# Kernel tuning notes

Hardware: AMD Instinct MI355X
Metric: run time of the kernel (lower is better)

The kernel has to match this reference:

```python
import jax, jax.numpy as jnp
import numpy as np

EPS = 1e-9  # Dice BatchNorm epsilon

def _dice(x, alpha, mm, mv):
    # Keras BN(center=False, scale=False) in inference mode: (x - moving_mean) / sqrt(moving_var + eps)
    p = jax.nn.sigmoid((x - mm) * jax.lax.rsqrt(mv + EPS))
    return x * (p + alpha * (1.0 - p))

def setup_inputs() -> dict:
    key = jax.random.key(0)
    ks = jax.random.split(key, 8)
    B, T, E = 4096, 200, 12
    return {
        "query": jax.random.normal(ks[0], (B, 1, E), jnp.float32),
        "keys": jax.random.normal(ks[1], (B, T, E), jnp.float32),
        "mask": jnp.ones((B, T), dtype=bool),
        "W0": jax.random.normal(ks[2], (48, 80), jnp.float32) * (1.0 / np.sqrt(48)),
        "b0": jnp.zeros((80,), jnp.float32),
        "W1": jax.random.normal(ks[3], (80, 40), jnp.float32) * (1.0 / np.sqrt(80)),
        "b1": jnp.zeros((40,), jnp.float32),
        "alpha0": jax.random.uniform(ks[4], (80,), jnp.float32),
        "alpha1": jax.random.uniform(ks[5], (40,), jnp.float32),
        "mm0": jnp.zeros((80,), jnp.float32),
        "mv0": jnp.ones((80,), jnp.float32),
        "mm1": jnp.zeros((40,), jnp.float32),
        "mv1": jnp.ones((40,), jnp.float32),
        "atten_kernel": jax.random.normal(ks[6], (40, 1), jnp.float32) * (1.0 / np.sqrt(40)),
        "atten_bias": jnp.zeros((1,), jnp.float32),
    }

def reference(query, keys, mask, W0, b0, W1, b1, alpha0, alpha1,
              mm0, mv0, mm1, mv1, atten_kernel, atten_bias):
    B, T, E = keys.shape
    q = jnp.broadcast_to(query, (B, T, E))  # K.repeat_elements(query, T, 1)
    att = jnp.concatenate([q, keys, q - keys, q * keys], axis=-1)  # [B, T, 4E=48]
    h = _dice(jnp.einsum('bti,io->bto', att, W0) + b0, alpha0, mm0, mv0)  # [B,T,80]
    h = _dice(jnp.einsum('bti,io->bto', h, W1) + b1, alpha1, mm1, mv1)    # [B,T,40]
    score = jnp.einsum('bti,io->bto', h, atten_kernel) + atten_bias       # [B,T,1]
    scores = jnp.swapaxes(score, 1, 2)  # [B,1,T]
    # NOTE: original code computes tf.where(mask,...) but overwrites it and
    # matmuls the UNMASKED scores with keys (bug reproduced faithfully).
    return jnp.matmul(scores, keys)  # [B,1,E]
```

## Files before the change

kernel.cpp:

```cpp
#include <hip/hip_runtime.h>
#include <hip/hip_bf16.h>
#include <math.h>

#define B_TOT 4096
#define T_LEN 200
#define E_DIM 12
#define LOG2E 1.44269504088896340736f

typedef __attribute__((ext_vector_type(8))) short bf16x8;
typedef __attribute__((ext_vector_type(4))) float f32x4;
typedef unsigned short ushort_t;


__device__ inline unsigned short f2bf(float f) {
    union { float f; unsigned u; } x; x.f = f;
    unsigned r = x.u + 0x7FFFu + ((x.u >> 16) & 1u);
    return (unsigned short)(r >> 16);
}
__device__ inline unsigned pk_bf16(float a, float b) {
    float2 t; t.x = a; t.y = b;
    __hip_bfloat162 h = __float22bfloat162_rn(t);
    union { __hip_bfloat162 h; unsigned u; } cv; cv.h = h;
    return cv.u;
}

__global__ __launch_bounds__(256) void din_prep(
    const float* __restrict__ W0, const float* __restrict__ b0v,
    const float* __restrict__ W1, const float* __restrict__ b1v,
    const float* __restrict__ a0, const float* __restrict__ a1,
    const float* __restrict__ mm0, const float* __restrict__ mv0,
    const float* __restrict__ mm1, const float* __restrict__ mv1,
    const float* __restrict__ ak, const float* __restrict__ ab,
    void* __restrict__ wsv)
{
    unsigned char* wsb = (unsigned char*)wsv;
    ushort_t* w0e2 = (ushort_t*)wsb;
    ushort_t* wq   = (ushort_t*)(wsb + 5120);
    ushort_t* w1e  = (ushort_t*)(wsb + 10240);
    float* d0c = (float*)(wsb + 19456);
    float* d1c = (float*)(wsb + 20736);

    int idx = blockIdx.x * 256 + threadIdx.x;
    if (idx < 2560) {
        int n = idx >> 5, k = idx & 31;
        float v = 0.0f;
        if (k < 12)       v = W0[(12 + k) * 80 + n] - W0[(24 + k) * 80 + n];
        else if (k < 24)  v = W0[(36 + (k - 12)) * 80 + n];
        w0e2[n * 32 + k] = f2bf(v);
    } else if (idx < 5120) {
        int v2 = idx - 2560;
        int n = v2 >> 5, k = v2 & 31;
        float v = 0.0f;
        if (k < 12)       v = W0[k * 80 + n] + W0[(24 + k) * 80 + n];
        else if (k == 12) v = b0v[n];
        wq[n * 32 + k] = f2bf(v);
    } else if (idx < 9728) {
        int v2 = idx - 5120;
        int n = v2 / 96, k = v2 - n * 96;
        float v = 0.0f;
        if (n < 40) {
            if (k < 80)       v = W1[k * 40 + n];
            else if (k == 80) v = b1v[n];
        } else if (n == 40 && k == 80) {
            v = 1.0f;
        }
        w1e[n * 96 + k] = f2bf(v);
    } else if (idx < 10048) {
        int v2 = idx - 9728;
        int o = v2 >> 2, c = v2 & 3;
        float rs = rsqrtf(mv0[o] + 1e-9f) * LOG2E;
        float val = (c == 0) ? -rs : (c == 1) ? mm0[o] * rs : (c == 2) ? a0[o] : 1.0f - a0[o];
        d0c[o * 4 + c] = val;
    } else {
        int v2 = idx - 10048;
        int j = v2 >> 2, c = v2 & 3;
        float val = 0.0f;
        if (j < 40) {
            float rs = rsqrtf(mv1[j] + 1e-9f) * LOG2E;
            val = (c == 0) ? -rs : (c == 1) ? mm1[j] * rs : (c == 2) ? a1[j] * ak[j]
                                                          : (1.0f - a1[j]) * ak[j];
        } else if (j == 40 && c == 2) {
            val = ab[0];
        }
        d1c[j * 4 + c] = val;
    }
}

#define A0_STR 40
#define H_STR  104
#define W1_STR 104

__global__ __launch_bounds__(256, 3) void din_mfma(
    const float* __restrict__ query, const float* __restrict__ keys,
    const void* __restrict__ wsv, float* __restrict__ out)
{
    __shared__ __align__(16) ushort_t Aseg[4 * 64];
    __shared__ __align__(16) ushort_t A0[4 * 64 * A0_STR];
    __shared__ __align__(16) ushort_t H[4 * 16 * H_STR];
    __shared__ __align__(16) f32x4 d0cL[80];
    __shared__ __align__(16) f32x4 d1cL[48];
    __shared__ __align__(16) ushort_t w1eL[48 * W1_STR];
    const unsigned char* wsb = (const unsigned char*)wsv;
    const ushort_t* w0e2 = (const ushort_t*)wsb;
    const ushort_t* wq   = (const ushort_t*)(wsb + 5120);
    const ushort_t* w1e  = (const ushort_t*)(wsb + 10240);
    const f32x4* d0cp = (const f32x4*)(wsb + 19456);
    const f32x4* d1cp = (const f32x4*)(wsb + 20736);

    const int tid = threadIdx.x;
    const int lane = tid & 63;
    const int w = tid >> 6;
    const int l15 = lane & 15;
    const int quad = lane >> 4;
    const int b = blockIdx.x * 4 + w;

    ushort_t* A0w = &A0[w * 64 * A0_STR];
    ushort_t* Hw  = &H[w * 16 * H_STR];
    ushort_t* Asw = &Aseg[w * 64];

    if (tid < 80)        d0cL[tid] = d0cp[tid];
    else if (tid < 128)  d1cL[tid - 80] = d1cp[tid - 80];
    for (int idx = tid; idx < 48 * 12; idx += 256) {
        int row = idx / 12, g = idx - row * 12;
        *(uint4*)(w1eL + row * W1_STR + g * 8) =
            *(const uint4*)(w1e + row * 96 + g * 8);
    }

    bf16x8 b0f[5];
    #pragma unroll
    for (int nt = 0; nt < 5; ++nt)
        b0f[nt] = *(const bf16x8*)(w0e2 + (nt * 16 + l15) * 32 + quad * 8);

    float qq[12];
    {
        const float4* qp = (const float4*)(query + (size_t)b * E_DIM);
        float4 q0 = qp[0], q1 = qp[1], q2 = qp[2];
        qq[0]=q0.x; qq[1]=q0.y; qq[2]=q0.z; qq[3]=q0.w;
        qq[4]=q1.x; qq[5]=q1.y; qq[6]=q1.z; qq[7]=q1.w;
        qq[8]=q2.x; qq[9]=q2.y; qq[10]=q2.z; qq[11]=q2.w;
    }

    float z0q[5];
    {
        unsigned p01 = pk_bf16(qq[0], qq[1]), p23 = pk_bf16(qq[2], qq[3]);
        unsigned p45 = pk_bf16(qq[4], qq[5]), p67 = pk_bf16(qq[6], qq[7]);
        unsigned p89 = pk_bf16(qq[8], qq[9]), pab = pk_bf16(qq[10], qq[11]);
        union { unsigned u[4]; bf16x8 v; } qa;
        qa.u[0] = (quad == 0) ? p01 : (quad == 1) ? p89 : 0u;
        qa.u[1] = (quad == 0) ? p23 : (quad == 1) ? pab : 0u;
        qa.u[2] = (quad == 0) ? p45 : (quad == 1) ? 0x00003F80u : 0u;
        qa.u[3] = (quad == 0) ? p67 : 0u;
        #pragma unroll
        for (int nt = 0; nt < 5; ++nt) {
            bf16x8 wf = *(const bf16x8*)(wq + (nt * 16 + l15) * 32 + quad * 8);
            f32x4 zz = {0.f, 0.f, 0.f, 0.f};
            zz = __builtin_amdgcn_mfma_f32_16x16x32_bf16(qa.v, wf, zz, 0, 0, 0);
            z0q[nt] = zz[0];
        }
    }

    if (quad == 0) {
        bf16x8 one8 = {(short)0x3F80, 0, 0, 0, 0, 0, 0, 0};
        bf16x8 zero8 = {0, 0, 0, 0, 0, 0, 0, 0};
        *(bf16x8*)(Hw + l15 * H_STR + 80) = one8;
        *(bf16x8*)(Hw + l15 * H_STR + 88) = zero8;
    }
    {
        uint4 z4; z4.x = 0u; z4.y = 0u; z4.z = 0u; z4.w = 0u;
        ((uint4*)(A0w + lane * A0_STR))[3] = z4;
    }

    __syncthreads();

    f32x4 acc2 = {0.f, 0.f, 0.f, 0.f};

    for (int c = 0; c < 4; ++c) {
        const int t0 = c * 64;
        const int myT = t0 + lane;
        const bool valid = myT < T_LEN;

        float kk[12];
        if (valid) {
            const float4* kp = (const float4*)(keys + ((size_t)b * T_LEN + myT) * E_DIM);
            float4 k0 = kp[0], k1 = kp[1], k2 = kp[2];
            kk[0]=k0.x; kk[1]=k0.y; kk[2]=k0.z; kk[3]=k0.w;
            kk[4]=k1.x; kk[5]=k1.y; kk[6]=k1.z; kk[7]=k1.w;
            kk[8]=k2.x; kk[9]=k2.y; kk[10]=k2.z; kk[11]=k2.w;
        } else {
            #pragma unroll
            for (int i = 0; i < 12; ++i) kk[i] = 0.0f;
        }
        {
            unsigned kw[6], qkw[6];
            #pragma unroll
            for (int i = 0; i < 6; ++i)
                kw[i] = pk_bf16(kk[2 * i], kk[2 * i + 1]);
            #pragma unroll
            for (int i = 0; i < 6; ++i)
                qkw[i] = pk_bf16(qq[2 * i] * kk[2 * i], qq[2 * i + 1] * kk[2 * i + 1]);
            uint4* dst = (uint4*)(A0w + lane * A0_STR);
            uint4 v0, v1, v2;
            v0.x = kw[0];  v0.y = kw[1];  v0.z = kw[2];  v0.w = kw[3];
            v1.x = kw[4];  v1.y = kw[5];  v1.z = qkw[0]; v1.w = qkw[1];
            v2.x = qkw[2]; v2.y = qkw[3]; v2.z = qkw[4]; v2.w = qkw[5];
            dst[0] = v0; dst[1] = v1; dst[2] = v2;
        }

        const int ntiles = (c < 3) ? 4 : 1;
        for (int ti = 0; ti < ntiles; ++ti) {
            bf16x8 a0 = *(const bf16x8*)(A0w + (ti * 16 + l15) * A0_STR + quad * 8);

            #pragma unroll
            for (int nt = 0; nt < 5; ++nt) {
                float zq = z0q[nt];
                f32x4 cc = {zq, zq, zq, zq};
                cc = __builtin_amdgcn_mfma_f32_16x16x32_bf16(a0, b0f[nt], cc, 0, 0, 0);
                f32x4 dc = d0cL[nt * 16 + l15];
                float h[4];
                #pragma unroll
                for (int r = 0; r < 4; ++r) {
                    float z = cc[r];
                    float pg = __builtin_amdgcn_rcpf(
                        1.0f + __builtin_amdgcn_exp2f(fmaf(z, dc.x, dc.y)));
                    h[r] = z * fmaf(pg, dc.w, dc.z);
                }
                unsigned u01 = pk_bf16(h[0], h[1]);
                unsigned u23 = pk_bf16(h[2], h[3]);
                ushort_t* hcol = Hw + (quad * 4) * H_STR + nt * 16 + l15;
                hcol[0 * H_STR] = (ushort_t)u01;
                hcol[1 * H_STR] = (ushort_t)(u01 >> 16);
                hcol[2 * H_STR] = (ushort_t)u23;
                hcol[3 * H_STR] = (ushort_t)(u23 >> 16);
            }

            bf16x8 af[3];
            #pragma unroll
            for (int ks = 0; ks < 3; ++ks)
                af[ks] = *(const bf16x8*)(Hw + l15 * H_STR + ks * 32 + quad * 8);
            float s[4] = {0.f, 0.f, 0.f, 0.f};
            #pragma unroll
            for (int nt = 0; nt < 3; ++nt) {
                f32x4 cc = {0.f, 0.f, 0.f, 0.f};
                #pragma unroll
                for (int ks = 0; ks < 3; ++ks) {
                    bf16x8 bf = *(const bf16x8*)(w1eL + (nt * 16 + l15) * W1_STR
                                                 + ks * 32 + quad * 8);
                    cc = __builtin_amdgcn_mfma_f32_16x16x32_bf16(af[ks], bf, cc, 0, 0, 0);
                }
                f32x4 dc1 = d1cL[nt * 16 + l15];
                #pragma unroll
                for (int r = 0; r < 4; ++r) {
                    float z = cc[r];
                    float pg = __builtin_amdgcn_rcpf(
                        1.0f + __builtin_amdgcn_exp2f(fmaf(z, dc1.x, dc1.y)));
                    s[r] = fmaf(z, fmaf(pg, dc1.w, dc1.z), s[r]);
                }
            }
            #pragma unroll
            for (int m = 1; m < 16; m <<= 1) {
                #pragma unroll
                for (int r = 0; r < 4; ++r) s[r] += __shfl_xor(s[r], m, 64);
            }
            if (l15 == 0) {
                const int tb = t0 + ti * 16 + quad * 4;
                float v0 = (tb + 0 < T_LEN) ? s[0] : 0.0f;
                float v1 = (tb + 1 < T_LEN) ? s[1] : 0.0f;
                float v2 = (tb + 2 < T_LEN) ? s[2] : 0.0f;
                float v3 = (tb + 3 < T_LEN) ? s[3] : 0.0f;
                unsigned lo = pk_bf16(v0, v1), hi = pk_bf16(v2, v3);
                unsigned long long pk = (unsigned long long)lo
                                      | ((unsigned long long)hi << 32);
                *(unsigned long long*)(Asw + ti * 16 + quad * 4) = pk;
            }
        }

        const int nks = (c < 3) ? 2 : 1;
        for (int ks = 0; ks < nks; ++ks) {
            bf16x8 pa = *(const bf16x8*)(Asw + l15 * 64 + ks * 32 + quad * 8);
            bf16x8 bk;
            #pragma unroll
            for (int j = 0; j < 8; ++j)
                bk[j] = (short)A0w[(ks * 32 + quad * 8 + j) * A0_STR + l15];
            acc2 = __builtin_amdgcn_mfma_f32_16x16x32_bf16(pa, bk, acc2, 0, 0, 0);
        }
    }

    if (quad == 0 && l15 < 12)
        out[(size_t)b * E_DIM + l15] = acc2[0];
}

extern "C" void kernel_launch(void* const* d_in, const int* in_sizes, int n_in,
                              void* d_out, int out_size, void* d_ws, size_t ws_size,
                              hipStream_t stream) {
    const float* query = (const float*)d_in[0];
    const float* keys  = (const float*)d_in[1];
    const float* W0  = (const float*)d_in[3];
    const float* b0v = (const float*)d_in[4];
    const float* W1  = (const float*)d_in[5];
    const float* b1v = (const float*)d_in[6];
    const float* a0  = (const float*)d_in[7];
    const float* a1  = (const float*)d_in[8];
    const float* mm0 = (const float*)d_in[9];
    const float* mv0 = (const float*)d_in[10];
    const float* mm1 = (const float*)d_in[11];
    const float* mv1 = (const float*)d_in[12];
    const float* ak  = (const float*)d_in[13];
    const float* ab  = (const float*)d_in[14];
    float* out = (float*)d_out;

    hipLaunchKernelGGL(din_prep, dim3(40), dim3(256), 0, stream,
                       W0, b0v, W1, b1v, a0, a1, mm0, mv0, mm1, mv1, ak, ab, d_ws);
    hipLaunchKernelGGL(din_mfma, dim3(B_TOT / 4), dim3(256), 0, stream,
                       query, keys, d_ws, out);
}
```

Baseline: 150.0 us.

## Process two 16-row tiles per iteration and keep W1 fragments in registers

The tile loop now handles pairs of 16-token tiles, interleaving two independent MFMA and Dice chains to hide MFMA latency. Each wave gets a double-buffered H scratch region. The W1 B-fragments are preloaded into registers instead of being staged in shared memory and re-read every tile. The extra register pressure lowers the launch bound from 3 to 2 blocks per CU, and the last chunk computes a redundant B tile whose result is discarded.

After: 152.5 us. Within noise of the previous version (+1.6%).

```diff
diff --git a/kernel.cpp b/kernel.cpp
--- a/kernel.cpp
+++ b/kernel.cpp
@@ -88,18 +88,16 @@
 
 #define A0_STR 40
 #define H_STR  104
-#define W1_STR 104
-
-__global__ __launch_bounds__(256, 3) void din_mfma(
+
+__global__ __launch_bounds__(256, 2) void din_mfma(
     const float* __restrict__ query, const float* __restrict__ keys,
     const void* __restrict__ wsv, float* __restrict__ out)
 {
     __shared__ __align__(16) ushort_t Aseg[4 * 64];
     __shared__ __align__(16) ushort_t A0[4 * 64 * A0_STR];
-    __shared__ __align__(16) ushort_t H[4 * 16 * H_STR];
+    __shared__ __align__(16) ushort_t H[4 * 2 * 16 * H_STR];
     __shared__ __align__(16) f32x4 d0cL[80];
     __shared__ __align__(16) f32x4 d1cL[48];
-    __shared__ __align__(16) ushort_t w1eL[48 * W1_STR];
     const unsigned char* wsb = (const unsigned char*)wsv;
     const ushort_t* w0e2 = (const ushort_t*)wsb;
     const ushort_t* wq   = (const ushort_t*)(wsb + 5120);
@@ -115,21 +113,23 @@
     const int b = blockIdx.x * 4 + w;
 
     ushort_t* A0w = &A0[w * 64 * A0_STR];
-    ushort_t* Hw  = &H[w * 16 * H_STR];
+    ushort_t* HwA = &H[(w * 2 + 0) * 16 * H_STR];
+    ushort_t* HwB = &H[(w * 2 + 1) * 16 * H_STR];
     ushort_t* Asw = &Aseg[w * 64];
 
     if (tid < 80)        d0cL[tid] = d0cp[tid];
     else if (tid < 128)  d1cL[tid - 80] = d1cp[tid - 80];
-    for (int idx = tid; idx < 48 * 12; idx += 256) {
-        int row = idx / 12, g = idx - row * 12;
-        *(uint4*)(w1eL + row * W1_STR + g * 8) =
-            *(const uint4*)(w1e + row * 96 + g * 8);
-    }
 
     bf16x8 b0f[5];
     #pragma unroll
     for (int nt = 0; nt < 5; ++nt)
         b0f[nt] = *(const bf16x8*)(w0e2 + (nt * 16 + l15) * 32 + quad * 8);
+    bf16x8 b1f[3][3];
+    #pragma unroll
+    for (int nt = 0; nt < 3; ++nt)
+        #pragma unroll
+        for (int ks = 0; ks < 3; ++ks)
+            b1f[nt][ks] = *(const bf16x8*)(w1e + (nt * 16 + l15) * 96 + ks * 32 + quad * 8);
 
     float qq[12];
     {
@@ -162,8 +162,10 @@
     if (quad == 0) {
         bf16x8 one8 = {(short)0x3F80, 0, 0, 0, 0, 0, 0, 0};
         bf16x8 zero8 = {0, 0, 0, 0, 0, 0, 0, 0};
-        *(bf16x8*)(Hw + l15 * H_STR + 80) = one8;
-        *(bf16x8*)(Hw + l15 * H_STR + 88) = zero8;
+        *(bf16x8*)(HwA + l15 * H_STR + 80) = one8;
+        *(bf16x8*)(HwA + l15 * H_STR + 88) = zero8;
+        *(bf16x8*)(HwB + l15 * H_STR + 80) = one8;
+        *(bf16x8*)(HwB + l15 * H_STR + 88) = zero8;
     }
     {
         uint4 z4; z4.x = 0u; z4.y = 0u; z4.z = 0u; z4.w = 0u;
@@ -206,71 +208,106 @@
             dst[0] = v0; dst[1] = v1; dst[2] = v2;
         }
 
-        const int ntiles = (c < 3) ? 4 : 1;
-        for (int ti = 0; ti < ntiles; ++ti) {
-            bf16x8 a0 = *(const bf16x8*)(A0w + (ti * 16 + l15) * A0_STR + quad * 8);
+        const int npairs = (c < 3) ? 2 : 1;
+        for (int pp = 0; pp < npairs; ++pp) {
+            const int tA = 2 * pp;
+            const int tB = (c < 3) ? (2 * pp + 1) : 0;
+            const bool writeB = (c < 3);
+
+            bf16x8 aA = *(const bf16x8*)(A0w + (tA * 16 + l15) * A0_STR + quad * 8);
+            bf16x8 aB = *(const bf16x8*)(A0w + (tB * 16 + l15) * A0_STR + quad * 8);
 
             #pragma unroll
             for (int nt = 0; nt < 5; ++nt) {
                 float zq = z0q[nt];
-                f32x4 cc = {zq, zq, zq, zq};
-                cc = __builtin_amdgcn_mfma_f32_16x16x32_bf16(a0, b0f[nt], cc, 0, 0, 0);
+                f32x4 cA = {zq, zq, zq, zq};
+                f32x4 cB = {zq, zq, zq, zq};
+                cA = __builtin_amdgcn_mfma_f32_16x16x32_bf16(aA, b0f[nt], cA, 0, 0, 0);
+                cB = __builtin_amdgcn_mfma_f32_16x16x32_bf16(aB, b0f[nt], cB, 0, 0, 0);
                 f32x4 dc = d0cL[nt * 16 + l15];
-                float h[4];
+                float hA[4], hB[4];
                 #pragma unroll
                 for (int r = 0; r < 4; ++r) {
-                    float z = cc[r];
-                    float pg = __builtin_amdgcn_rcpf(
-                        1.0f + __builtin_amdgcn_exp2f(fmaf(z, dc.x, dc.y)));
-                    h[r] = z * fmaf(pg, dc.w, dc.z);
-                }
-                unsigned u01 = pk_bf16(h[0], h[1]);
-                unsigned u23 = pk_bf16(h[2], h[3]);
-                ushort_t* hcol = Hw + (quad * 4) * H_STR + nt * 16 + l15;
-                hcol[0 * H_STR] = (ushort_t)u01;
-                hcol[1 * H_STR] = (ushort_t)(u01 >> 16);
-                hcol[2 * H_STR] = (ushort_t)u23;
-                hcol[3 * H_STR] = (ushort_t)(u23 >> 16);
-            }
-
-            bf16x8 af[3];
-            #pragma unroll
-            for (int ks = 0; ks < 3; ++ks)
-                af[ks] = *(const bf16x8*)(Hw + l15 * H_STR + ks * 32 + quad * 8);
-            float s[4] = {0.f, 0.f, 0.f, 0.f};
+                    float zA = cA[r], zB = cB[r];
+                    float pA = __builtin_amdgcn_rcpf(
+                        1.0f + __builtin_amdgcn_exp2f(fmaf(zA, dc.x, dc.y)));
+                    float pB = __builtin_amdgcn_rcpf(
+                        1.0f + __builtin_amdgcn_exp2f(fmaf(zB, dc.x, dc.y)));
+                    hA[r] = zA * fmaf(pA, dc.w, dc.z);
+                    hB[r] = zB * fmaf(pB, dc.w, dc.z);
+                }
+                unsigned a01 = pk_bf16(hA[0], hA[1]), a23 = pk_bf16(hA[2], hA[3]);
+                unsigned b01 = pk_bf16(hB[0], hB[1]), b23 = pk_bf16(hB[2], hB[3]);
+                ushort_t* hcA = HwA + (quad * 4) * H_STR + nt * 16 + l15;
+                ushort_t* hcB = HwB + (quad * 4) * H_STR + nt * 16 + l15;
+                hcA[0 * H_STR] = (ushort_t)a01;
+                hcA[1 * H_STR] = (ushort_t)(a01 >> 16);
+                hcA[2 * H_STR] = (ushort_t)a23;
+                hcA[3 * H_STR] = (ushort_t)(a23 >> 16);
+                hcB[0 * H_STR] = (ushort_t)b01;
+                hcB[1 * H_STR] = (ushort_t)(b01 >> 16);
+                hcB[2 * H_STR] = (ushort_t)b23;
+                hcB[3 * H_STR] = (ushort_t)(b23 >> 16);
+            }
+
+            bf16x8 afA[3], afB[3];
+            #pragma unroll
+            for (int ks = 0; ks < 3; ++ks) {
+                afA[ks] = *(const bf16x8*)(HwA + l15 * H_STR + ks * 32 + quad * 8);
+                afB[ks] = *(const bf16x8*)(HwB + l15 * H_STR + ks * 32 + quad * 8);
+            }
+            float sA[4] = {0.f, 0.f, 0.f, 0.f};
+            float sB[4] = {0.f, 0.f, 0.f, 0.f};
             #pragma unroll
             for (int nt = 0; nt < 3; ++nt) {
-                f32x4 cc = {0.f, 0.f, 0.f, 0.f};
+                f32x4 cA = {0.f, 0.f, 0.f, 0.f};
+                f32x4 cB = {0.f, 0.f, 0.f, 0.f};
                 #pragma unroll
                 for (int ks = 0; ks < 3; ++ks) {
-                    bf16x8 bf = *(const bf16x8*)(w1eL + (nt * 16 + l15) * W1_STR
-                                                 + ks * 32 + quad * 8);
-                    cc = __builtin_amdgcn_mfma_f32_16x16x32_bf16(af[ks], bf, cc, 0, 0, 0);
+                    cA = __builtin_amdgcn_mfma_f32_16x16x32_bf16(afA[ks], b1f[nt][ks], cA, 0, 0, 0);
+                    cB = __builtin_amdgcn_mfma_f32_16x16x32_bf16(afB[ks], b1f[nt][ks], cB, 0, 0, 0);
                 }
                 f32x4 dc1 = d1cL[nt * 16 + l15];
                 #pragma unroll
                 for (int r = 0; r < 4; ++r) {
-                    float z = cc[r];
-                    float pg = __builtin_amdgcn_rcpf(
-                        1.0f + __builtin_amdgcn_exp2f(fmaf(z, dc1.x, dc1.y)));
-                    s[r] = fmaf(z, fmaf(pg, dc1.w, dc1.z), s[r]);
+                    float zA = cA[r], zB = cB[r];
+                    float pA = __builtin_amdgcn_rcpf(
+                        1.0f + __builtin_amdgcn_exp2f(fmaf(zA, dc1.x, dc1.y)));
+                    float pB = __builtin_amdgcn_rcpf(
+                        1.0f + __builtin_amdgcn_exp2f(fmaf(zB, dc1.x, dc1.y)));
+                    sA[r] = fmaf(zA, fmaf(pA, dc1.w, dc1.z), sA[r]);
+                    sB[r] = fmaf(zB, fmaf(pB, dc1.w, dc1.z), sB[r]);
                 }
             }
             #pragma unroll
             for (int m = 1; m < 16; m <<= 1) {
                 #pragma unroll
-                for (int r = 0; r < 4; ++r) s[r] += __shfl_xor(s[r], m, 64);
+                for (int r = 0; r < 4; ++r) {
+                    sA[r] += __shfl_xor(sA[r], m, 64);
+                    sB[r] += __shfl_xor(sB[r], m, 64);
+                }
             }
             if (l15 == 0) {
-                const int tb = t0 + ti * 16 + quad * 4;
-                float v0 = (tb + 0 < T_LEN) ? s[0] : 0.0f;
-                float v1 = (tb + 1 < T_LEN) ? s[1] : 0.0f;
-                float v2 = (tb + 2 < T_LEN) ? s[2] : 0.0f;
-                float v3 = (tb + 3 < T_LEN) ? s[3] : 0.0f;
-                unsigned lo = pk_bf16(v0, v1), hi = pk_bf16(v2, v3);
-                unsigned long long pk = (unsigned long long)lo
-                                      | ((unsigned long long)hi << 32);
-                *(unsigned long long*)(Asw + ti * 16 + quad * 4) = pk;
+                {
+                    const int tb = t0 + tA * 16 + quad * 4;
+                    float v0 = (tb + 0 < T_LEN) ? sA[0] : 0.0f;
+                    float v1 = (tb + 1 < T_LEN) ? sA[1] : 0.0f;
+                    float v2 = (tb + 2 < T_LEN) ? sA[2] : 0.0f;
+                    float v3 = (tb + 3 < T_LEN) ? sA[3] : 0.0f;
+                    unsigned lo = pk_bf16(v0, v1), hi = pk_bf16(v2, v3);
+                    *(unsigned long long*)(Asw + tA * 16 + quad * 4) =
+                        (unsigned long long)lo | ((unsigned long long)hi << 32);
+                }
+                if (writeB) {
+                    const int tb = t0 + tB * 16 + quad * 4;
+                    float v0 = (tb + 0 < T_LEN) ? sB[0] : 0.0f;
+                    float v1 = (tb + 1 < T_LEN) ? sB[1] : 0.0f;
+                    float v2 = (tb + 2 < T_LEN) ? sB[2] : 0.0f;
+                    float v3 = (tb + 3 < T_LEN) ? sB[3] : 0.0f;
+                    unsigned lo = pk_bf16(v0, v1), hi = pk_bf16(v2, v3);
+                    *(unsigned long long*)(Asw + tB * 16 + quad * 4) =
+                        (unsigned long long)lo | ((unsigned long long)hi << 32);
+                }
             }
         }
 
```
